# Performance work log

Hardware: AMD Instinct MI355X
Metric: run time of the kernel (lower is better)

The kernel has to match this reference:

```python
import jax, jax.numpy as jnp
import numpy as np


def setup_inputs() -> dict:
    key = jax.random.key(0)
    k1, k2, k3, k4, k5 = jax.random.split(key, 5)
    B, S, DK, D = 64, 2048, 1024, 1024
    hidden_state = jax.random.normal(k1, (B, D), dtype=jnp.float32)
    encoder_outputs = jax.random.normal(k2, (B, S, DK), dtype=jnp.float32)
    # linear1: in = dim_key + dim*num_layers = 2048, out = dim = 1024
    W1 = jax.random.normal(k3, (D, DK + D), dtype=jnp.float32) * (1.0 / np.sqrt(DK + D))
    b1 = jax.random.normal(k4, (D,), dtype=jnp.float32) * 0.01
    W2 = jax.random.normal(k5, (1, D), dtype=jnp.float32) * (1.0 / np.sqrt(D))
    return {"hidden_state": hidden_state, "encoder_outputs": encoder_outputs,
            "W1": W1, "b1": b1, "W2": W2}


def reference(hidden_state, encoder_outputs, W1, b1, W2):
    # torch: cat([enc, h], -1) @ W1.T  ==  enc @ W1e.T + h @ W1h.T
    # (split avoids materializing the [B,S,DK+D] concat; same math)
    DK = encoder_outputs.shape[-1]
    W1e, W1h = W1[:, :DK], W1[:, DK:]
    # pre: [B, S, D]
    pre = (jnp.einsum('bsk,dk->bsd', encoder_outputs, W1e)
           + jnp.einsum('bm,dm->bd', hidden_state, W1h)[:, None, :]
           + b1)
    e = jnp.einsum('bsd,d->bs', jnp.tanh(pre), W2[0])  # scores [B, S]
    alpha = jax.nn.softmax(e, axis=1)
    context = jnp.einsum('bs,bsk->bk', alpha, encoder_outputs)  # [B, DK]
    return context
```

## Files before the change

kernel.cpp:

```cpp
#include <hip/hip_runtime.h>

typedef __attribute__((ext_vector_type(8))) short short8;
typedef __attribute__((ext_vector_type(4))) float floatx4;

#define M_TOT 131072
#define SEQ   2048
#define NB    8

__device__ __forceinline__ unsigned bf16rne(float x) {
  unsigned u = __float_as_uint(x);
  return (u + 0x7FFFu + ((u >> 16) & 1u)) >> 16;
}

#define GLOAD_LDS16(g, l) __builtin_amdgcn_global_load_lds( \
    (const __attribute__((address_space(1))) unsigned int*)(g), \
    (__attribute__((address_space(3))) unsigned int*)(l), 16, 0, 0)

__global__ __launch_bounds__(256) void convert_enc_kernel(
    const float* __restrict__ in, unsigned int* __restrict__ out)
{
  size_t i = ((size_t)blockIdx.x * 256 + threadIdx.x) * 8;
  float4 a = *(const float4*)(in + i);
  float4 b = *(const float4*)(in + i + 4);
  uint4 o;
  o.x = bf16rne(a.x) | (bf16rne(a.y) << 16);
  o.y = bf16rne(a.z) | (bf16rne(a.w) << 16);
  o.z = bf16rne(b.x) | (bf16rne(b.y) << 16);
  o.w = bf16rne(b.z) | (bf16rne(b.w) << 16);
  *(uint4*)(out + i / 2) = o;
}

__global__ __launch_bounds__(128) void convert_w1e_kernel(
    const float* __restrict__ W1, unsigned int* __restrict__ out)
{
  int d = blockIdx.x;
  int k = threadIdx.x * 8;
  const float* p = W1 + (size_t)d * 2048 + k;
  float4 a = *(const float4*)p;
  float4 b = *(const float4*)(p + 4);
  uint4 o;
  o.x = bf16rne(a.x) | (bf16rne(a.y) << 16);
  o.y = bf16rne(a.z) | (bf16rne(a.w) << 16);
  o.z = bf16rne(b.x) | (bf16rne(b.y) << 16);
  o.w = bf16rne(b.z) | (bf16rne(b.w) << 16);
  *(uint4*)(out + ((size_t)d * 1024 + k) / 2) = o;
}

__global__ __launch_bounds__(256) void hvec_kernel(
    const float* __restrict__ hid, const float* __restrict__ W1,
    const float* __restrict__ b1, float* __restrict__ hvec)
{
  int b = blockIdx.x, g = blockIdx.y;
  int w = threadIdx.x >> 6, lane = threadIdx.x & 63;
  const float* hrow = hid + b * 1024;
  for (int i = 0; i < 16; ++i) {
    int d = g * 64 + w * 16 + i;
    const float* wrow = W1 + (size_t)d * 2048 + 1024;
    float sum = 0.f;
#pragma unroll
    for (int c = 0; c < 4; ++c) {
      int m = c * 256 + lane * 4;
      float4 wv = *(const float4*)(wrow + m);
      float4 hv = *(const float4*)(hrow + m);
      sum += wv.x * hv.x + wv.y * hv.y + wv.z * hv.z + wv.w * hv.w;
    }
#pragma unroll
    for (int msk = 1; msk < 64; msk <<= 1) sum += __shfl_xor(sum, msk);
    if (lane == 0) hvec[b * 1024 + d] = sum + b1[d];
  }
}

__global__ __launch_bounds__(256) void gemm_bf16_kernel(
    const unsigned short* __restrict__ A, const unsigned short* __restrict__ B,
    const float* __restrict__ W2, const float* __restrict__ hvec,
    float* __restrict__ epart)
{
  __shared__ __align__(16) unsigned short Ah[128 * 32];
  __shared__ __align__(16) unsigned short Bh[128 * 32];
  __shared__ float ep[2][128];

  const int tid = threadIdx.x;
  const int nb = blockIdx.x;
  const int mb = blockIdx.y;
  const int r0 = mb * 128, n0 = nb * 128;
  const int bidx = r0 >> 11;
  const int w = tid >> 6, lane = tid & 63;
  const int wm = w >> 1, wn = w & 1;
  const int lrow = lane & 15, kq = lane >> 4;

  floatx4 acc[4][4];
#pragma unroll
  for (int i = 0; i < 4; ++i)
#pragma unroll
    for (int j = 0; j < 4; ++j)
      acc[i][j] = (floatx4){0.f, 0.f, 0.f, 0.f};

  const unsigned short* aBase = A + (size_t)r0 * 1024;
  const unsigned short* bBase = B + (size_t)n0 * 1024;

  for (int k0 = 0; k0 < 1024; k0 += 32) {
    __syncthreads();
#pragma unroll
    for (int j = 0; j < 2; ++j) {
      int c = tid + j * 256;
      int row = c >> 2, kc = c & 3;
      const unsigned short* ag = aBase + (size_t)row * 1024 + k0 + kc * 8;
      const unsigned short* bg = bBase + (size_t)row * 1024 + k0 + kc * 8;
      int ldsbase = (w * 64 + j * 256) * 8;
      GLOAD_LDS16(ag, &Ah[ldsbase]);
      GLOAD_LDS16(bg, &Bh[ldsbase]);
    }
    __syncthreads();

    short8 af[4], bfm[4];
#pragma unroll
    for (int t4 = 0; t4 < 4; ++t4) {
      af[t4]  = *(const short8*)&Ah[(wm * 64 + t4 * 16 + lrow) * 32 + kq * 8];
      bfm[t4] = *(const short8*)&Bh[(wn * 64 + t4 * 16 + lrow) * 32 + kq * 8];
    }
#pragma unroll
    for (int mt = 0; mt < 4; ++mt)
#pragma unroll
      for (int nt = 0; nt < 4; ++nt)
        acc[mt][nt] = __builtin_amdgcn_mfma_f32_16x16x32_bf16(
            af[mt], bfm[nt], acc[mt][nt], 0, 0, 0);
  }

  float hv[4], w2v[4];
#pragma unroll
  for (int nt = 0; nt < 4; ++nt) {
    int n = n0 + wn * 64 + nt * 16 + lrow;
    hv[nt]  = hvec[bidx * 1024 + n];
    w2v[nt] = W2[n];
  }
#pragma unroll
  for (int mt = 0; mt < 4; ++mt) {
#pragma unroll
    for (int r = 0; r < 4; ++r) {
      float sum = 0.f;
#pragma unroll
      for (int nt = 0; nt < 4; ++nt) {
        float pre = acc[mt][nt][r] + hv[nt];
        float ex = __expf(2.f * pre);
        sum += (1.f - 2.f / (ex + 1.f)) * w2v[nt];
      }
      sum += __shfl_xor(sum, 1);
      sum += __shfl_xor(sum, 2);
      sum += __shfl_xor(sum, 4);
      sum += __shfl_xor(sum, 8);
      if (lrow == 0) ep[wn][wm * 64 + mt * 16 + kq * 4 + r] = sum;
    }
  }
  __syncthreads();
  if (tid < 128)
    epart[(size_t)nb * M_TOT + r0 + tid] = ep[0][tid] + ep[1][tid];
}

__global__ __launch_bounds__(256) void fused_gemm_kernel(
    const float* __restrict__ enc, const float* __restrict__ W1,
    const float* __restrict__ W2, const float* __restrict__ hvec,
    float* __restrict__ epart)
{
  __shared__ __align__(16) unsigned short Ah[128 * 32];
  __shared__ __align__(16) unsigned short Bh[128 * 32];
  __shared__ float ep[2][128];

  const int tid = threadIdx.x;
  const int nb = blockIdx.x, mb = blockIdx.y;
  const int r0 = mb * 128, n0 = nb * 128;
  const int bidx = r0 >> 11;
  const int w = tid >> 6, lane = tid & 63;
  const int wm = w >> 1, wn = w & 1;
  const int lrow = lane & 15, kq = lane >> 4;

  floatx4 acc[4][4];
#pragma unroll
  for (int i = 0; i < 4; ++i)
#pragma unroll
    for (int j = 0; j < 4; ++j)
      acc[i][j] = (floatx4){0.f, 0.f, 0.f, 0.f};

  const int srow = tid >> 3;
  const int scol = (tid & 7) * 4;
  const float* aptr = enc + (size_t)(r0 + srow) * 1024 + scol;
  const float* bptr = W1  + (size_t)(n0 + srow) * 2048 + scol;

  for (int k0 = 0; k0 < 1024; k0 += 32) {
    float4 av[4], bv[4];
#pragma unroll
    for (int j = 0; j < 4; ++j) {
      av[j] = *(const float4*)(aptr + (size_t)(j * 32) * 1024 + k0);
      bv[j] = *(const float4*)(bptr + (size_t)(j * 32) * 2048 + k0);
    }
    __syncthreads();
#pragma unroll
    for (int j = 0; j < 4; ++j) {
      unsigned ax = __float_as_uint(av[j].x), ay = __float_as_uint(av[j].y);
      unsigned az = __float_as_uint(av[j].z), aw = __float_as_uint(av[j].w);
      unsigned a01 = __builtin_amdgcn_perm(ay, ax, 0x07060302u);
      unsigned a23 = __builtin_amdgcn_perm(aw, az, 0x07060302u);
      *(uint2*)&Ah[(tid + j * 256) * 4] = make_uint2(a01, a23);
      unsigned bx = __float_as_uint(bv[j].x), by = __float_as_uint(bv[j].y);
      unsigned bz = __float_as_uint(bv[j].z), bw = __float_as_uint(bv[j].w);
      unsigned b01 = __builtin_amdgcn_perm(by, bx, 0x07060302u);
      unsigned b23 = __builtin_amdgcn_perm(bw, bz, 0x07060302u);
      *(uint2*)&Bh[(tid + j * 256) * 4] = make_uint2(b01, b23);
    }
    __syncthreads();

    short8 af[4], bfm[4];
#pragma unroll
    for (int t4 = 0; t4 < 4; ++t4) {
      af[t4]  = *(const short8*)&Ah[(wm * 64 + t4 * 16 + lrow) * 32 + kq * 8];
      bfm[t4] = *(const short8*)&Bh[(wn * 64 + t4 * 16 + lrow) * 32 + kq * 8];
    }
#pragma unroll
    for (int mt = 0; mt < 4; ++mt)
#pragma unroll
      for (int nt = 0; nt < 4; ++nt)
        acc[mt][nt] = __builtin_amdgcn_mfma_f32_16x16x32_bf16(
            af[mt], bfm[nt], acc[mt][nt], 0, 0, 0);
  }

  float hv[4], w2v[4];
#pragma unroll
  for (int nt = 0; nt < 4; ++nt) {
    int n = n0 + wn * 64 + nt * 16 + lrow;
    hv[nt]  = hvec[bidx * 1024 + n];
    w2v[nt] = W2[n];
  }
#pragma unroll
  for (int mt = 0; mt < 4; ++mt) {
#pragma unroll
    for (int r = 0; r < 4; ++r) {
      float sum = 0.f;
#pragma unroll
      for (int nt = 0; nt < 4; ++nt) {
        float pre = acc[mt][nt][r] + hv[nt];
        float ex = __expf(2.f * pre);
        sum += (1.f - 2.f / (ex + 1.f)) * w2v[nt];
      }
      sum += __shfl_xor(sum, 1);
      sum += __shfl_xor(sum, 2);
      sum += __shfl_xor(sum, 4);
      sum += __shfl_xor(sum, 8);
      if (lrow == 0) ep[wn][wm * 64 + mt * 16 + kq * 4 + r] = sum;
    }
  }
  __syncthreads();
  if (tid < 128)
    epart[(size_t)nb * M_TOT + r0 + tid] = ep[0][tid] + ep[1][tid];
}

__global__ __launch_bounds__(256) void softmax_kernel(
    const float* __restrict__ epart, float* __restrict__ alpha)
{
  int b = blockIdx.x, t = threadIdx.x;
  __shared__ float redmax[4], redsum[4];
  float ev[8];
  float lmax = -1e30f;
#pragma unroll
  for (int j = 0; j < 8; ++j) {
    int s = t + j * 256;
    float sum = 0.f;
#pragma unroll
    for (int p = 0; p < 8; ++p) sum += epart[(size_t)p * M_TOT + b * SEQ + s];
    ev[j] = sum;
    lmax = fmaxf(lmax, sum);
  }
#pragma unroll
  for (int msk = 1; msk < 64; msk <<= 1) lmax = fmaxf(lmax, __shfl_xor(lmax, msk));
  if ((t & 63) == 0) redmax[t >> 6] = lmax;
  __syncthreads();
  float bmax = fmaxf(fmaxf(redmax[0], redmax[1]), fmaxf(redmax[2], redmax[3]));
  float lsum = 0.f;
#pragma unroll
  for (int j = 0; j < 8; ++j) { ev[j] = __expf(ev[j] - bmax); lsum += ev[j]; }
#pragma unroll
  for (int msk = 1; msk < 64; msk <<= 1) lsum += __shfl_xor(lsum, msk);
  if ((t & 63) == 0) redsum[t >> 6] = lsum;
  __syncthreads();
  float inv = 1.f / (redsum[0] + redsum[1] + redsum[2] + redsum[3]);
#pragma unroll
  for (int j = 0; j < 8; ++j) alpha[b * SEQ + t + j * 256] = ev[j] * inv;
}

__global__ __launch_bounds__(128) void context_bf16_kernel(
    const unsigned int* __restrict__ encB, const float* __restrict__ alpha,
    float* __restrict__ out)
{
  int b = blockIdx.x, sc = blockIdx.y, t = threadIdx.x;
  int k8 = t * 8;
  const unsigned int* ep = encB + (((size_t)b * SEQ + sc * 64) * 1024 + k8) / 2;
  const float* ap = alpha + b * SEQ + sc * 64;
  float a0 = 0.f, a1 = 0.f, a2 = 0.f, a3 = 0.f, a4 = 0.f, a5 = 0.f, a6 = 0.f, a7 = 0.f;
#pragma unroll 4
  for (int s = 0; s < 64; ++s) {
    float a = ap[s];
    uint4 v = *(const uint4*)(ep + (size_t)s * 512);
    a0 += a * __uint_as_float(v.x << 16);
    a1 += a * __uint_as_float(v.x & 0xFFFF0000u);
    a2 += a * __uint_as_float(v.y << 16);
    a3 += a * __uint_as_float(v.y & 0xFFFF0000u);
    a4 += a * __uint_as_float(v.z << 16);
    a5 += a * __uint_as_float(v.z & 0xFFFF0000u);
    a6 += a * __uint_as_float(v.w << 16);
    a7 += a * __uint_as_float(v.w & 0xFFFF0000u);
  }
  float* o = out + b * 1024 + k8;
  atomicAdd(o + 0, a0); atomicAdd(o + 1, a1);
  atomicAdd(o + 2, a2); atomicAdd(o + 3, a3);
  atomicAdd(o + 4, a4); atomicAdd(o + 5, a5);
  atomicAdd(o + 6, a6); atomicAdd(o + 7, a7);
}

__global__ __launch_bounds__(256) void context_kernel(
    const float* __restrict__ enc, const float* __restrict__ alpha,
    float* __restrict__ out)
{
  int b = blockIdx.y, sq = blockIdx.z, t = threadIdx.x;
  int k4 = t * 4;
  const float* ep = enc + ((size_t)b * SEQ + sq * 128) * 1024 + k4;
  const float* ap = alpha + b * SEQ + sq * 128;
  float ax = 0.f, ay = 0.f, az = 0.f, aw = 0.f;
#pragma unroll 4
  for (int s = 0; s < 128; ++s) {
    float a = ap[s];
    float4 v = *(const float4*)(ep + (size_t)s * 1024);
    ax += a * v.x; ay += a * v.y; az += a * v.z; aw += a * v.w;
  }
  float* o = out + b * 1024 + k4;
  atomicAdd(o + 0, ax);
  atomicAdd(o + 1, ay);
  atomicAdd(o + 2, az);
  atomicAdd(o + 3, aw);
}

extern "C" void kernel_launch(void* const* d_in, const int* in_sizes, int n_in,
                              void* d_out, int out_size, void* d_ws, size_t ws_size,
                              hipStream_t stream) {
  const float* hid = (const float*)d_in[0];
  const float* enc = (const float*)d_in[1];
  const float* W1  = (const float*)d_in[2];
  const float* b1  = (const float*)d_in[3];
  const float* W2  = (const float*)d_in[4];
  float* out = (float*)d_out;

  float* epart = (float*)d_ws;
  float* alpha = epart + (size_t)NB * M_TOT;
  float* hvec  = alpha + M_TOT;
  size_t small_bytes = ((size_t)NB * M_TOT + M_TOT + 64 * 1024) * 4;
  size_t encB_off = ((small_bytes + 255) / 256) * 256;
  size_t need = encB_off + (size_t)M_TOT * 1024 * 2 + (size_t)1024 * 1024 * 2;

  hipMemsetAsync(d_out, 0, (size_t)out_size * sizeof(float), stream);
  hvec_kernel<<<dim3(64, 16), 256, 0, stream>>>(hid, W1, b1, hvec);

  if (ws_size >= need) {
    unsigned short* encB = (unsigned short*)((char*)d_ws + encB_off);
    unsigned short* W1eB = encB + (size_t)M_TOT * 1024;
    convert_enc_kernel<<<65536, 256, 0, stream>>>(enc, (unsigned int*)encB);
    convert_w1e_kernel<<<1024, 128, 0, stream>>>(W1, (unsigned int*)W1eB);
    gemm_bf16_kernel<<<dim3(NB, 1024), 256, 0, stream>>>(encB, W1eB, W2, hvec, epart);
    softmax_kernel<<<64, 256, 0, stream>>>(epart, alpha);
    context_bf16_kernel<<<dim3(64, 32), 128, 0, stream>>>((unsigned int*)encB, alpha, out);
  } else {
    fused_gemm_kernel<<<dim3(NB, 1024), 256, 0, stream>>>(enc, W1, W2, hvec, epart);
    softmax_kernel<<<64, 256, 0, stream>>>(epart, alpha);
    context_kernel<<<dim3(1, 64, 16), 256, 0, stream>>>(enc, alpha, out);
  }
}
```

Measured before the change: 1.270 ms.

## Swizzle GEMM blocks per XCD and restructure context reduction without atomics

Remaps the GEMM block index so each XCD gets a contiguous range of row blocks and all eight column blocks for a row tile, aiming to improve L2 reuse of the A rows. The context kernel now splits work by 128-column chunks with 8 sequence strips per block, reduced in shared memory and written directly. This removes the float atomics and the output memset on the bf16 path. Each thread now reads narrower 8-byte loads over longer strips, and only 512 blocks launch, which may reduce memory-level parallelism.

```diff
diff --git a/kernel.cpp b/kernel.cpp
--- a/kernel.cpp
+++ b/kernel.cpp
@@ -80,8 +80,11 @@
   __shared__ float ep[2][128];
 
   const int tid = threadIdx.x;
-  const int nb = blockIdx.x;
-  const int mb = blockIdx.y;
+  const int lid = blockIdx.x + blockIdx.y * 8;
+  const int xcd = lid & 7;
+  const int q   = lid >> 3;
+  const int mb  = (xcd << 7) + (q >> 3);
+  const int nb  = q & 7;
   const int r0 = mb * 128, n0 = nb * 128;
   const int bidx = r0 >> 11;
   const int w = tid >> 6, lane = tid & 63;
@@ -285,33 +288,38 @@
   for (int j = 0; j < 8; ++j) alpha[b * SEQ + t + j * 256] = ev[j] * inv;
 }
 
-__global__ __launch_bounds__(128) void context_bf16_kernel(
+__global__ __launch_bounds__(256) void context_bf16_kernel(
     const unsigned int* __restrict__ encB, const float* __restrict__ alpha,
     float* __restrict__ out)
 {
-  int b = blockIdx.x, sc = blockIdx.y, t = threadIdx.x;
-  int k8 = t * 8;
-  const unsigned int* ep = encB + (((size_t)b * SEQ + sc * 64) * 1024 + k8) / 2;
-  const float* ap = alpha + b * SEQ + sc * 64;
-  float a0 = 0.f, a1 = 0.f, a2 = 0.f, a3 = 0.f, a4 = 0.f, a5 = 0.f, a6 = 0.f, a7 = 0.f;
+  __shared__ float red[8][128];
+  int b = blockIdx.x, kc = blockIdx.y, t = threadIdx.x;
+  int kl = (t & 31) * 4;
+  int strip = t >> 5;
+  const unsigned int* ep = encB +
+      (((size_t)b * SEQ + strip * 256) * 1024 + kc * 128 + kl) / 2;
+  const float* ap = alpha + b * SEQ + strip * 256;
+  float a0 = 0.f, a1 = 0.f, a2 = 0.f, a3 = 0.f;
 #pragma unroll 4
-  for (int s = 0; s < 64; ++s) {
+  for (int s = 0; s < 256; ++s) {
     float a = ap[s];
-    uint4 v = *(const uint4*)(ep + (size_t)s * 512);
+    uint2 v = *(const uint2*)(ep + (size_t)s * 512);
     a0 += a * __uint_as_float(v.x << 16);
     a1 += a * __uint_as_float(v.x & 0xFFFF0000u);
     a2 += a * __uint_as_float(v.y << 16);
     a3 += a * __uint_as_float(v.y & 0xFFFF0000u);
-    a4 += a * __uint_as_float(v.z << 16);
-    a5 += a * __uint_as_float(v.z & 0xFFFF0000u);
-    a6 += a * __uint_as_float(v.w << 16);
-    a7 += a * __uint_as_float(v.w & 0xFFFF0000u);
-  }
-  float* o = out + b * 1024 + k8;
-  atomicAdd(o + 0, a0); atomicAdd(o + 1, a1);
-  atomicAdd(o + 2, a2); atomicAdd(o + 3, a3);
-  atomicAdd(o + 4, a4); atomicAdd(o + 5, a5);
-  atomicAdd(o + 6, a6); atomicAdd(o + 7, a7);
+  }
+  red[strip][kl + 0] = a0;
+  red[strip][kl + 1] = a1;
+  red[strip][kl + 2] = a2;
+  red[strip][kl + 3] = a3;
+  __syncthreads();
+  if (t < 128) {
+    float s = 0.f;
+#pragma unroll
+    for (int j = 0; j < 8; ++j) s += red[j][t];
+    out[b * 1024 + kc * 128 + t] = s;
+  }
 }
 
 __global__ __launch_bounds__(256) void context_kernel(
@@ -353,7 +361,6 @@
   size_t encB_off = ((small_bytes + 255) / 256) * 256;
   size_t need = encB_off + (size_t)M_TOT * 1024 * 2 + (size_t)1024 * 1024 * 2;
 
-  hipMemsetAsync(d_out, 0, (size_t)out_size * sizeof(float), stream);
   hvec_kernel<<<dim3(64, 16), 256, 0, stream>>>(hid, W1, b1, hvec);
 
   if (ws_size >= need) {
@@ -363,8 +370,9 @@
     convert_w1e_kernel<<<1024, 128, 0, stream>>>(W1, (unsigned int*)W1eB);
     gemm_bf16_kernel<<<dim3(NB, 1024), 256, 0, stream>>>(encB, W1eB, W2, hvec, epart);
     softmax_kernel<<<64, 256, 0, stream>>>(epart, alpha);
-    context_bf16_kernel<<<dim3(64, 32), 128, 0, stream>>>((unsigned int*)encB, alpha, out);
+    context_bf16_kernel<<<dim3(64, 8), 256, 0, stream>>>((unsigned int*)encB, alpha, out);
   } else {
+    hipMemsetAsync(d_out, 0, (size_t)out_size * sizeof(float), stream);
     fused_gemm_kernel<<<dim3(NB, 1024), 256, 0, stream>>>(enc, W1, W2, hvec, epart);
     softmax_kernel<<<64, 256, 0, stream>>>(epart, alpha);
     context_kernel<<<dim3(1, 64, 16), 256, 0, stream>>>(enc, alpha, out);
```

After: 1.160 ms. 8.7% less time.
